# Kernel optimization log

Measured on AMD Instinct MI355X. Metric: run time of the kernel, lower is better.

Reference implementation:

```python
import jax, jax.numpy as jnp
import numpy as np

T_STEPS = 4000          # T_ms / dt = 1000 / 0.25
N_IN, N_OUT = 64, 10
HID = [1024, 1024]
DT, TAU = 0.25, 10.0
BETA = float(np.exp(-DT / TAU))   # beta_snn
THR = 1.0                          # thr_snn
SLOPE = 1.0                        # spike_snn uses slope=1.0
W_STD = 32.0                       # W_STD_CUBA

@jax.custom_vjp
def spike(u):
    # SurrogateSpike.forward: heaviside on (mem - thr)
    return (u >= 0).astype(u.dtype)

def _spike_fwd(u):
    return spike(u), u

def _spike_bwd(u, g):
    # fast-sigmoid surrogate: slope / (1 + slope*|u|)^2
    grad = SLOPE / (1.0 + SLOPE * jnp.abs(u)) ** 2
    return (g * grad,)

spike.defvjp(_spike_fwd, _spike_bwd)

def setup_inputs() -> dict:
    key = jax.random.key(0)
    ks = jax.random.split(key, 8)
    B = 16
    # Bernoulli(0.05) input spike train, time-major [T, B, N_IN]
    input_spikes = (jax.random.uniform(ks[0], (T_STEPS, B, N_IN)) < 0.05).astype(jnp.float32)
    sizes = [N_IN] + HID + [N_OUT]
    inp = {"input_spikes": input_spikes}
    for i, (n_pre, n_post) in enumerate(zip(sizes[:-1], sizes[1:])):
        # init_weight 'normal': clamp(N(0, W_STD), min=0) / n_pre
        w = jnp.maximum(jax.random.normal(ks[i + 1], (n_pre, n_post)) * W_STD, 0.0) / n_pre
        inp[f"W{i}"] = w.astype(jnp.float32)
        inp[f"b{i}"] = jnp.zeros((n_post,), jnp.float32)
    return inp

def reference(input_spikes, W0, b0, W1, b1, W2, b2):
    # Dale's law: feedforward weights clamped >= 0 in forward
    Ws = [jnp.maximum(W, 0.0) for W in (W0, W1, W2)]
    bs = [b0, b1, b2]
    B = input_spikes.shape[1]
    sizes = HID + [N_OUT]
    mems0 = tuple(jnp.zeros((B, n), input_spikes.dtype) for n in sizes)

    def step(mems, s_in):
        s = s_in
        new_mems = []
        for l in range(len(Ws)):
            I = s @ Ws[l] + bs[l]                 # [B, n_post]
            m = BETA * mems[l] + I                # LIF decay + drive
            sp = spike(m - THR)                   # surrogate-grad spike
            m = jnp.where(sp > 0, 0.0, m)         # hard reset to zero
            new_mems.append(m)
            s = sp
        return tuple(new_mems), s                 # emit output-layer spikes

    _, out_spikes = jax.lax.scan(step, mems0, input_spikes)
    return out_spikes  # [T, B, N_OUT]
```

## Files before the change

### kernel.cpp

```cpp
#include <hip/hip_runtime.h>
#include <hip/hip_bf16.h>
#include <math.h>


#define T_STEPS 4000
#define NB 16
#define N_IN 64
#define NH 1024
#define N_OUT 10
#define SEGO 40
#define SEGH 40

typedef __attribute__((ext_vector_type(8))) short bf16x8;
typedef __attribute__((ext_vector_type(4))) float f32x4;
typedef __hip_bfloat16 bf16;
typedef unsigned long long u64;

#define ASG(p) (const __attribute__((address_space(1))) void*)(p)
#define ASL(p) (__attribute__((address_space(3))) void*)(p)


__global__ __launch_bounds__(256) void k_prep(
    const float* __restrict__ in_sp, u64* __restrict__ mask,
    const float* __restrict__ W1, bf16* __restrict__ BT1,
    const float* __restrict__ W2, bf16* __restrict__ BT2,
    float* __restrict__ mst, int nM, int ZB, int MB) {
    __shared__ float Wlds[64][65];
    int b = blockIdx.x;
    const int tid = threadIdx.x;
    if (b < ZB) {
        int i = b * 256 + tid;
        if (i < nM) mst[i] = 0.f;
        return;
    }
    b -= ZB;
    if (b < MB) {
        int w = b * 4 + (tid >> 6);
        int lane = tid & 63;
        float v = in_sp[(size_t)w * 64 + lane];
        u64 bal = __ballot(v > 0.5f);
        if (lane == 0) mask[w] = bal;
        return;
    }
    b -= MB;
    if (b < 256) {
        const int lane = tid & 63;
        const int wr   = tid >> 6;
        const int k0 = (b & 15) * 64;
        const int n0 = (b >> 4) * 64;
#pragma unroll
        for (int rr = 0; rr < 16; ++rr) {
            int kl = wr * 16 + rr;
            Wlds[kl][lane] = W1[(size_t)(k0 + kl) * 1024 + n0 + lane];
        }
        __syncthreads();
#pragma unroll
        for (int rr = 0; rr < 16; ++rr) {
            int nl = wr * 16 + rr;
            float w = fmaxf(Wlds[lane][nl], 0.f);
            bf16 h = __float2bfloat16(w);
            float hf = __bfloat162float(h);
            bf16 l = __float2bfloat16(w - hf);
            size_t base = (size_t)(n0 + nl) * 2048 + k0 + lane;
            BT1[base] = h;
            BT1[base + 1024] = l;
        }
        return;
    }
    b -= 256;
    {
        int idx = b * 256 + tid;
        int total = 128 * 2 * NH;
        if (idx >= total) return;
        int n  = idx / (2 * NH);
        int k2 = idx - n * (2 * NH);
        int lo = (k2 >= NH);
        int k = lo ? (k2 - NH) : k2;
        float v = 0.f;
        if (n < N_OUT) {
            float w = fmaxf(W2[(size_t)k * N_OUT + n], 0.f);
            float hi = __bfloat162float(__float2bfloat16(w));
            v = lo ? (w - hi) : w;
        }
        BT2[idx] = __float2bfloat16(v);
    }
}

__global__ void k_unpack(const u64* __restrict__ BITS, float* __restrict__ out,
                         int total) {
    int idx = blockIdx.x * 256 + threadIdx.x;
    if (idx >= total) return;
    int t   = idx / (NB * N_OUT);
    int rem = idx - t * (NB * N_OUT);
    int b = rem / N_OUT;
    int k = rem - b * N_OUT;
    u64 w = BITS[(size_t)(t / SEGO) * 256 + b * 16 + k];
    out[idx] = ((w >> (t % SEGO)) & 1ULL) ? 1.f : 0.f;
}


__device__ __forceinline__ void scan_out_body(
    const float* __restrict__ I2, const float* __restrict__ bias,
    float* __restrict__ mstate, u64* __restrict__ BITS,
    int Tc, float* seg, int tid) {
    float* segA = seg;
    float* segB = seg + SEGO * 256;
    const bool act = tid < 256;
    const int lane = tid & 63;
    const int wave = tid >> 6;
    const int k = tid & 15;
    float m = 0.f, bj = 0.f;
    if (act) {
        m = mstate[tid];
        bj = (k < N_OUT) ? bias[k] : 0.f;
    }
    const int nseg = Tc / SEGO;

#define O_PREFETCH(SEGBUF, SIDX)                                            \
    if (act) {                                                              \
        const float* src = I2 + (size_t)(SIDX) * SEGO * 256                 \
                              + (size_t)wave * 256 + lane * 4;              \
        _Pragma("unroll")                                                   \
        for (int g = 0; g < SEGO / 4; ++g)                                  \
            __builtin_amdgcn_global_load_lds(                               \
                ASG(src + (size_t)(g * 4) * 256),                           \
                ASL(&SEGBUF[(g * 4 + wave) * 256]), 16, 0, 0);              \
    }

#define O_PROC(SEGBUF, SIDX)                                                \
    if (act) {                                                              \
        u64 obits = 0;                                                      \
        _Pragma("unroll")                                                   \
        for (int sb = 0; sb < SEGO / 8; ++sb) {                             \
            float v[8];                                                     \
            _Pragma("unroll")                                               \
            for (int u = 0; u < 8; ++u)                                     \
                v[u] = SEGBUF[(sb * 8 + u) * 256 + tid];                    \
            _Pragma("unroll")                                               \
            for (int u = 0; u < 8; ++u) {                                   \
                m = fmaf(beta_c, m, v[u] + bj);                             \
                bool sp = (m >= 1.0f);                                      \
                obits |= ((u64)(sp ? 1 : 0)) << (sb * 8 + u);               \
                m = sp ? 0.f : m;                                           \
            }                                                               \
        }                                                                   \
        BITS[(size_t)(SIDX) * 256 + tid] = obits;                           \
    }

    const float beta_c = 0.97530991202833261687f;
    O_PREFETCH(segA, 0);
    O_PREFETCH(segB, 1);
    asm volatile("s_waitcnt vmcnt(10)" ::: "memory");
    __builtin_amdgcn_sched_barrier(0);
    __builtin_amdgcn_s_barrier();
    for (int s = 0; s < nseg; s += 2) {
        O_PROC(segA, s);
        if (s + 2 < nseg) {
            O_PREFETCH(segA, s + 2);
            asm volatile("s_waitcnt vmcnt(11)" ::: "memory");
        } else {
            asm volatile("s_waitcnt vmcnt(1)" ::: "memory");
        }
        __builtin_amdgcn_sched_barrier(0);
        __builtin_amdgcn_s_barrier();
        O_PROC(segB, s + 1);
        if (s + 3 < nseg) {
            O_PREFETCH(segB, s + 3);
            asm volatile("s_waitcnt vmcnt(11)" ::: "memory");
            __builtin_amdgcn_sched_barrier(0);
            __builtin_amdgcn_s_barrier();
        } else if (s + 2 < nseg) {
            asm volatile("s_waitcnt vmcnt(1)" ::: "memory");
            __builtin_amdgcn_sched_barrier(0);
            __builtin_amdgcn_s_barrier();
        }
    }
    if (act) mstate[tid] = m;
#undef O_PREFETCH
#undef O_PROC
}

__global__ __launch_bounds__(256) void k_scan_out(
    const float* __restrict__ I2, const float* __restrict__ bias,
    float* __restrict__ mstate, u64* __restrict__ BITS, int Tc) {
    __shared__ __align__(16) float seg[2 * SEGO * 256];
    scan_out_body(I2, bias, mstate, BITS, Tc, seg, threadIdx.x);
}


__global__ __launch_bounds__(256) void k_gemm_thin(
    const bf16* __restrict__ A, const bf16* __restrict__ BT,
    float* __restrict__ C) {
    const int tid  = threadIdx.x;
    const int lane = tid & 63;
    const int wave = tid >> 6;
    const int r16 = lane & 15;
    const int kg  = lane >> 4;
    const int m0 = blockIdx.x * 64 + wave * 16;
    f32x4 acc = {};
    const bf16* ap = A + (size_t)(m0 + r16) * 1024 + kg * 8;
    const bf16* bh = BT + (size_t)r16 * 2048 + kg * 8;
    const bf16* bl = bh + 1024;
#pragma unroll 8
    for (int kt = 0; kt < 32; ++kt) {
        const int ka = kt * 32;
        bf16x8 af  = *(const bf16x8*)(ap + ka);
        bf16x8 bfh = *(const bf16x8*)(bh + ka);
        bf16x8 bfl = *(const bf16x8*)(bl + ka);
        acc = __builtin_amdgcn_mfma_f32_16x16x32_bf16(af, bfh, acc, 0, 0, 0);
        acc = __builtin_amdgcn_mfma_f32_16x16x32_bf16(af, bfl, acc, 0, 0, 0);
    }
#pragma unroll
    for (int rr = 0; rr < 4; ++rr)
        C[(size_t)(m0 + kg * 4 + rr) * 16 + r16] = acc[rr];
}


__global__ __launch_bounds__(512) void k_gemm8(
    const bf16* __restrict__ A, const bf16* __restrict__ BT,
    float* __restrict__ C, int gx,
    const float* __restrict__ I2t, const float* __restrict__ b2t,
    float* __restrict__ m2t, u64* __restrict__ BITSt, int tcT, int doTail) {
    __shared__ __align__(16) char LDS[131072];
    const int tid  = threadIdx.x;

    if (doTail && (int)blockIdx.x == (int)gridDim.x - 1) {
        scan_out_body(I2t, b2t, m2t, BITSt, tcT, (float*)LDS, tid);
        return;
    }

    const int KA = 1024, K2 = 2048;
    const int kmask = KA - 1;
    const int nwg = gridDim.x - doTail;
    const int wg  = blockIdx.x;
    const int q = nwg >> 3, r = nwg & 7;
    const int xcd = wg & 7, idx0 = wg >> 3;
    const int swz = (xcd < r ? xcd * (q + 1) : r * (q + 1) + (xcd - r) * q) + idx0;
    const int gy = nwg / gx;
    const int n0 = (swz % gy) * 256;
    const int m0 = (swz / gy) * 256;

    const int lane = tid & 63;
    const int wave = tid >> 6;
    const int wm = (wave >> 2) * 128;
    const int wn = (wave & 3) * 64;
    const int r16l = lane & 15;
    const int kg   = lane >> 4;
    const int hA   = wave >> 2;
    const int hB   = (wave & 3) >> 1;
    const int wn64 = wave & 1;

    const int po = (r16l * 64 + kg * 16) ^ (((r16l >> 3) & 1) << 5);
    const char* bA[2] = { LDS + hA * 16384 + po,
                          LDS + 65536 + hA * 16384 + po };
    const char* bB[2] = { LDS + 32768 + hB * 16384 + po,
                          LDS + 98304 + hB * 16384 + po };
    const int bOff = wn64 * 8192;

    int s_row[2], s_col[2];
#pragma unroll
    for (int rr = 0; rr < 2; ++rr) {
        int d = (rr * 512 + tid) * 16;
        int l = d ^ (((d >> 9) & 1) << 5);
        int sub = l >> 10;
        int w = l & 1023;
        s_row[rr] = (sub >> 1) * 16 + (w >> 6);
        s_col[rr] = ((sub & 1) * 64 + (w & 63)) >> 1;
    }

#define HBASE(BUF, OP, HALF) ((((BUF) * 2 + (OP)) * 2 + (HALF)) * 16384)
#define STAGE_A(BUF, HALF, K0)                                              \
    {                                                                       \
        _Pragma("unroll")                                                   \
        for (int rr = 0; rr < 2; ++rr)                                      \
            __builtin_amdgcn_global_load_lds(                               \
                ASG(A + (size_t)(m0 + (HALF) * 128 + s_row[rr]) * KA        \
                    + (((K0) + s_col[rr]) & kmask)),                        \
                ASL(LDS + HBASE(BUF, 0, HALF) + (rr * 512 + wave * 64) * 16), \
                16, 0, 0);                                                  \
    }
#define STAGE_B(BUF, HALF, K0)                                              \
    {                                                                       \
        _Pragma("unroll")                                                   \
        for (int rr = 0; rr < 2; ++rr)                                      \
            __builtin_amdgcn_global_load_lds(                               \
                ASG(BT + (size_t)(n0 + (HALF) * 128 + s_row[rr]) * K2       \
                    + (K0) + s_col[rr]),                                    \
                ASL(LDS + HBASE(BUF, 1, HALF) + (rr * 512 + wave * 64) * 16), \
                16, 0, 0);                                                  \
    }

    f32x4 acc[8][4] = {};
    bf16x8 a[4][2], b[4][2];

#define MM(MIB, NIB)                                                        \
    {                                                                       \
        _Pragma("unroll")                                                   \
        for (int i = 0; i < 4; ++i)                                         \
            _Pragma("unroll")                                               \
            for (int j = 0; j < 2; ++j) {                                   \
                acc[(MIB) + i][(NIB) + j] =                                 \
                    __builtin_amdgcn_mfma_f32_16x16x32_bf16(                \
                        a[i][0], b[(NIB) + j][0], acc[(MIB) + i][(NIB) + j], 0, 0, 0); \
                acc[(MIB) + i][(NIB) + j] =                                 \
                    __builtin_amdgcn_mfma_f32_16x16x32_bf16(                \
                        a[i][1], b[(NIB) + j][1], acc[(MIB) + i][(NIB) + j], 0, 0, 0); \
            }                                                               \
    }

#define PH_SYNC()                                                           \
    __builtin_amdgcn_s_barrier();                                           \
    asm volatile("s_waitcnt lgkmcnt(0)" ::: "memory");                      \
    __builtin_amdgcn_sched_barrier(0);

#define KTILE(BUF, SK)                                                      \
    {                                                                       \
        _Pragma("unroll")                                                   \
        for (int i = 0; i < 4; ++i) {                                       \
            a[i][0] = *(const bf16x8*)(bA[BUF] + i * 2048);                 \
            a[i][1] = *(const bf16x8*)(bA[BUF] + i * 2048 + 1024);          \
        }                                                                   \
        _Pragma("unroll")                                                   \
        for (int j = 0; j < 2; ++j) {                                       \
            b[j][0] = *(const bf16x8*)(bB[BUF] + bOff + j * 2048);          \
            b[j][1] = *(const bf16x8*)(bB[BUF] + bOff + j * 2048 + 1024);   \
        }                                                                   \
        PH_SYNC();                                                          \
        __builtin_amdgcn_s_setprio(1);                                      \
        MM(0, 0);                                                           \
        __builtin_amdgcn_s_setprio(0);                                      \
        __builtin_amdgcn_s_barrier();                                       \
        _Pragma("unroll")                                                   \
        for (int j = 0; j < 2; ++j) {                                       \
            b[2 + j][0] = *(const bf16x8*)(bB[BUF] + bOff + (2 + j) * 2048); \
            b[2 + j][1] = *(const bf16x8*)(bB[BUF] + bOff + (2 + j) * 2048 + 1024); \
        }                                                                   \
        PH_SYNC();                                                          \
        __builtin_amdgcn_s_setprio(1);                                      \
        MM(0, 2);                                                           \
        __builtin_amdgcn_s_setprio(0);                                      \
        __builtin_amdgcn_s_barrier();                                       \
        _Pragma("unroll")                                                   \
        for (int i = 0; i < 4; ++i) {                                       \
            a[i][0] = *(const bf16x8*)(bA[BUF] + (4 + i) * 2048);           \
            a[i][1] = *(const bf16x8*)(bA[BUF] + (4 + i) * 2048 + 1024);    \
        }                                                                   \
        STAGE_B(BUF, 0, SK);                                                \
        STAGE_B(BUF, 1, SK);                                                \
        PH_SYNC();                                                          \
        __builtin_amdgcn_s_setprio(1);                                      \
        MM(4, 0);                                                           \
        __builtin_amdgcn_s_setprio(0);                                      \
        __builtin_amdgcn_s_barrier();                                       \
        STAGE_A(BUF, 0, SK);                                                \
        STAGE_A(BUF, 1, SK);                                                \
        PH_SYNC();                                                          \
        __builtin_amdgcn_s_setprio(1);                                      \
        MM(4, 2);                                                           \
        __builtin_amdgcn_s_setprio(0);                                      \
        asm volatile("s_waitcnt vmcnt(8)" ::: "memory");                    \
        __builtin_amdgcn_sched_barrier(0);                                  \
        __builtin_amdgcn_s_barrier();                                       \
    }

    STAGE_A(0, 0, 0);  STAGE_A(0, 1, 0);  STAGE_B(0, 0, 0);  STAGE_B(0, 1, 0);
    STAGE_A(1, 0, 64); STAGE_A(1, 1, 64); STAGE_B(1, 0, 64); STAGE_B(1, 1, 64);
    asm volatile("s_waitcnt vmcnt(8)" ::: "memory");
    __builtin_amdgcn_sched_barrier(0);
    __builtin_amdgcn_s_barrier();

    for (int it = 0; it < 16; ++it) {
        const int k0  = it * 128;
        const int ksA = (k0 + 128) & (K2 - 1);
        const int ksB = (k0 + 192) & (K2 - 1);
        KTILE(0, ksA);
        KTILE(1, ksB);
    }
    asm volatile("s_waitcnt vmcnt(0)" ::: "memory");
    __builtin_amdgcn_sched_barrier(0);

#pragma unroll
    for (int mi = 0; mi < 8; ++mi)
#pragma unroll
        for (int ni = 0; ni < 4; ++ni)
#pragma unroll
            for (int rr = 0; rr < 4; ++rr) {
                int row = m0 + wm + mi * 16 + kg * 4 + rr;
                int col = n0 + wn + ni * 16 + r16l;
                C[(size_t)row * 1024 + col] = acc[mi][ni][rr];
            }
#undef KTILE
#undef PH_SYNC
#undef MM
#undef STAGE_A
#undef STAGE_B
#undef HBASE
}


__global__ __launch_bounds__(64) void k_scan_l0(
    const u64* __restrict__ mask,
    const float* __restrict__ W0,
    const float* __restrict__ bias,
    float* __restrict__ mstate, bf16* __restrict__ S, int Tc, float beta) {
    __shared__ float Ilds[2][16][68];
    const int lane = threadIdx.x;
    const int gid  = blockIdx.x * 64 + lane;
    const int b  = blockIdx.x >> 4;
    const int q  = blockIdx.x & 15;
    const int j0 = q * 64;
    const int r16 = lane & 15;
    const int kg  = lane >> 4;
    bf16x8 bh[4][2], bl[4][2];
#pragma unroll
    for (int jt = 0; jt < 4; ++jt)
#pragma unroll
        for (int kk = 0; kk < 2; ++kk)
#pragma unroll
            for (int e = 0; e < 8; ++e) {
                int k = kk * 32 + kg * 8 + e;
                float w = fmaxf(W0[(size_t)k * 1024 + j0 + jt * 16 + r16], 0.f);
                bf16 h = __float2bfloat16(w);
                float hf = __bfloat162float(h);
                bf16 l = __float2bfloat16(w - hf);
                bh[jt][kk][e] = *(short*)&h;
                bl[jt][kk][e] = *(short*)&l;
            }
    float m = mstate[gid];
    const float bj = bias[j0 + lane];
    const size_t stride = (size_t)NB * NH;
    const int ntile = Tc / 16;
    const int tmax = ntile - 1;

#define LOADM(TT) mask[(size_t)(((TT) <= tmax ? (TT) : tmax) * 16 + r16) * NB + b]

#define L0_COMPUTE(MSK, P)                                                  \
    {                                                                       \
        f32x4 acc[4] = {};                                                  \
        _Pragma("unroll")                                                   \
        for (int kk = 0; kk < 2; ++kk) {                                    \
            unsigned byte8 = (unsigned)(((MSK) >> (kk * 32 + kg * 8)) & 0xFF); \
            bf16x8 af;                                                      \
            _Pragma("unroll")                                               \
            for (int e = 0; e < 8; ++e)                                     \
                af[e] = ((byte8 >> e) & 1) ? (short)0x3F80 : (short)0;      \
            _Pragma("unroll")                                               \
            for (int jt = 0; jt < 4; ++jt) {                                \
                acc[jt] = __builtin_amdgcn_mfma_f32_16x16x32_bf16(          \
                    af, bh[jt][kk], acc[jt], 0, 0, 0);                      \
                acc[jt] = __builtin_amdgcn_mfma_f32_16x16x32_bf16(          \
                    af, bl[jt][kk], acc[jt], 0, 0, 0);                      \
            }                                                               \
        }                                                                   \
        _Pragma("unroll")                                                   \
        for (int jt = 0; jt < 4; ++jt)                                      \
            _Pragma("unroll")                                               \
            for (int rr = 0; rr < 4; ++rr)                                  \
                Ilds[P][kg * 4 + rr][jt * 16 + r16] = acc[jt][rr];          \
    }

    u64 mc = LOADM(0);
    L0_COMPUTE(mc, 0);
    u64 mn = LOADM(1);
    for (int tt = 0; tt < ntile; ++tt) {
        __builtin_amdgcn_s_barrier();
        float v[16];
#pragma unroll
        for (int u = 0; u < 16; ++u)
            v[u] = Ilds[tt & 1][u][lane];
        u64 m2 = LOADM(tt + 2);
        if (tt + 1 < ntile) L0_COMPUTE(mn, (tt + 1) & 1);
        unsigned short o[16];
#pragma unroll
        for (int u = 0; u < 16; ++u) {
            m = fmaf(beta, m, v[u] + bj);
            bool sp = (m >= 1.0f);
            o[u] = sp ? (unsigned short)0x3F80 : (unsigned short)0;
            m = sp ? 0.f : m;
        }
#pragma unroll
        for (int u = 0; u < 16; ++u)
            ((unsigned short*)S)[(size_t)(tt * 16 + u) * stride + gid] = o[u];
        mn = m2;
    }
    mstate[gid] = m;
#undef L0_COMPUTE
#undef LOADM
}

__global__ __launch_bounds__(64) void k_scan_hidden(
    const float* __restrict__ I, const float* __restrict__ bias,
    float* __restrict__ mstate, bf16* __restrict__ S, int Tc, float beta) {
    __shared__ __align__(16) float segA[SEGH * 64];
    __shared__ __align__(16) float segB[SEGH * 64];
    const int lane = threadIdx.x;
    const int gid  = blockIdx.x * 64 + lane;
    const int j = gid & (NH - 1);
    float m = mstate[gid];
    const float bj = bias[j];
    const size_t stride = (size_t)NB * NH;
    const int nseg = Tc / SEGH;
    const int lrow = lane >> 4;
    const int lcol = (lane & 15) << 2;

#define H_PREFETCH(SEGBUF, SIDX)                                            \
    {                                                                       \
        const float* src = I + (size_t)(SIDX) * SEGH * stride               \
                             + (size_t)lrow * stride + blockIdx.x * 64 + lcol; \
        _Pragma("unroll")                                                   \
        for (int g = 0; g < SEGH / 4; ++g)                                  \
            __builtin_amdgcn_global_load_lds(                               \
                ASG(src + (size_t)(g * 4) * stride),                        \
                ASL(&SEGBUF[g * 256]), 16, 0, 0);                           \
    }

#define H_PROC(SEGBUF, SIDX)                                                \
    {                                                                       \
        const int btt = (SIDX) * SEGH;                                      \
        _Pragma("unroll")                                                   \
        for (int sb = 0; sb < SEGH / 8; ++sb) {                             \
            float v[8];                                                     \
            _Pragma("unroll")                                               \
            for (int u = 0; u < 8; ++u)                                     \
                v[u] = SEGBUF[(sb * 8 + u) * 64 + lane];                    \
            unsigned short o[8];                                            \
            _Pragma("unroll")                                               \
            for (int u = 0; u < 8; ++u) {                                   \
                m = fmaf(beta, m, v[u] + bj);                               \
                bool sp = (m >= 1.0f);                                      \
                o[u] = sp ? (unsigned short)0x3F80 : (unsigned short)0;     \
                m = sp ? 0.f : m;                                           \
            }                                                               \
            _Pragma("unroll")                                               \
            for (int u = 0; u < 8; ++u)                                     \
                ((unsigned short*)S)[(size_t)(btt + sb * 8 + u) * stride + gid] = o[u]; \
        }                                                                   \
    }

    H_PREFETCH(segA, 0);
    H_PREFETCH(segB, 1);
    asm volatile("s_waitcnt vmcnt(10)" ::: "memory");
    __builtin_amdgcn_sched_barrier(0);
    for (int s = 0; s < nseg; s += 2) {
        H_PROC(segA, s);
        if (s + 2 < nseg) {
            H_PREFETCH(segA, s + 2);
            asm volatile("s_waitcnt vmcnt(50)" ::: "memory");
        } else {
            asm volatile("s_waitcnt vmcnt(40)" ::: "memory");
        }
        __builtin_amdgcn_sched_barrier(0);
        H_PROC(segB, s + 1);
        if (s + 3 < nseg) {
            H_PREFETCH(segB, s + 3);
            asm volatile("s_waitcnt vmcnt(50)" ::: "memory");
            __builtin_amdgcn_sched_barrier(0);
        } else if (s + 2 < nseg) {
            asm volatile("s_waitcnt vmcnt(40)" ::: "memory");
            __builtin_amdgcn_sched_barrier(0);
        }
    }
    mstate[gid] = m;
#undef H_PREFETCH
#undef H_PROC
}


extern "C" void kernel_launch(void* const* d_in, const int* in_sizes, int n_in,
                              void* d_out, int out_size, void* d_ws, size_t ws_size,
                              hipStream_t stream) {
    const float* in_sp = (const float*)d_in[0];
    const float* W0 = (const float*)d_in[1];
    const float* b0 = (const float*)d_in[2];
    const float* W1 = (const float*)d_in[3];
    const float* b1 = (const float*)d_in[4];
    const float* W2 = (const float*)d_in[5];
    const float* b2 = (const float*)d_in[6];
    float* out = (float*)d_out;

    char* p = (char*)d_ws;
    auto carve = [&](size_t bytes) -> void* {
        char* r = p; p += (bytes + 255) & ~(size_t)255; return (void*)r;
    };
    u64*  MASK  = (u64*)carve((size_t)T_STEPS * NB * 8);
    bf16* BT1   = (bf16*)carve((size_t)NH * 2 * NH * 2);
    bf16* BT2   = (bf16*)carve((size_t)128 * 2 * NH * 2);
    float* m0s  = (float*)carve((size_t)NB * NH * 4);
    float* m1s  = (float*)carve((size_t)NB * NH * 4);
    float* m2s  = (float*)carve((size_t)NB * 16 * 4);
    float* I2BUF = (float*)carve((size_t)T_STEPS * NB * 16 * 4);
    u64*  BITS  = (u64*)carve((size_t)(T_STEPS / SEGO) * 256 * 8);
    size_t fixed = (size_t)(p - (char*)d_ws);

    const int tc_opts[3] = {2000, 800, 400};
    int Tc = 400;
    for (int i = 0; i < 3; ++i) {
        size_t Mc_ = (size_t)tc_opts[i] * NB;
        size_t need = fixed
            + ((Mc_ * NH * 4 + 255) & ~(size_t)255)
            + ((Mc_ * NH * 2 + 255) & ~(size_t)255);
        if (need <= ws_size) { Tc = tc_opts[i]; break; }
    }
    size_t Mc = (size_t)Tc * NB;
    float* IBUF = (float*)carve(Mc * NH * 4);
    bf16*  S    = (bf16*)carve(Mc * NH * 2);

    const float beta = (float)exp(-0.25 / 10.0);

    int nM = NB * NH * 2 + NB * 16;
    const int ZB = (nM + 255) / 256;
    const int MB = (T_STEPS * NB) / 4;
    const int L2B = (128 * 2 * NH + 255) / 256;
    k_prep<<<ZB + MB + 256 + L2B, 256, 0, stream>>>(
        in_sp, MASK, W1, BT1, W2, BT2, m0s, nM, ZB, MB);

    const int C = T_STEPS / Tc;
    const int gx8 = (int)(Mc / 256);
    const int gthin = (int)(Mc / 64);
    for (int c = 0; c < C; ++c) {
        int t0 = c * Tc;
        k_scan_l0<<<256, 64, 0, stream>>>(MASK + (size_t)t0 * NB, W0, b0,
                                          m0s, S, Tc, beta);
        if (c == 0) {
            k_gemm8<<<gx8 * 4, 512, 0, stream>>>(S, BT1, IBUF, gx8,
                                                 nullptr, nullptr, nullptr,
                                                 nullptr, 0, 0);
        } else {
            int tp = (c - 1) * Tc;
            k_gemm8<<<gx8 * 4 + 1, 512, 0, stream>>>(
                S, BT1, IBUF, gx8,
                I2BUF + (size_t)tp * NB * 16, b2, m2s,
                BITS + (size_t)(tp / SEGO) * 256, Tc, 1);
        }
        k_scan_hidden<<<(NB * NH) / 64, 64, 0, stream>>>(IBUF, b1, m1s, S, Tc, beta);
        k_gemm_thin<<<gthin, 256, 0, stream>>>(S, BT2,
                                               I2BUF + (size_t)t0 * NB * 16);
    }
    int tl = (C - 1) * Tc;
    k_scan_out<<<1, 256, 0, stream>>>(I2BUF + (size_t)tl * NB * 16, b2, m2s,
                                      BITS + (size_t)(tl / SEGO) * 256, Tc);
    int nOut = T_STEPS * NB * N_OUT;
    k_unpack<<<(nOut + 255) / 256, 256, 0, stream>>>(BITS, out, nOut);
}
```

Measured before the change: 672.1 us.

## Interleave hi/lo weight K-blocks so each A tile is reused across both halves

The split-bf16 weight matrix is reordered so the hi and lo halves of each 64-wide K block sit next to each other. The GEMM main loop then loads each A tile once into LDS and reuses it for two consecutive B tiles (hi, then lo), instead of reloading A for the second half of K. This roughly halves A-side global-to-LDS traffic. In exchange the LDS buffering scheme and wait counts become more intricate, with separate even and odd k-tile macros.

```diff
diff --git a/kernel.cpp b/kernel.cpp
--- a/kernel.cpp
+++ b/kernel.cpp
@@ -61,9 +61,9 @@
             bf16 h = __float2bfloat16(w);
             float hf = __bfloat162float(h);
             bf16 l = __float2bfloat16(w - hf);
-            size_t base = (size_t)(n0 + nl) * 2048 + k0 + lane;
+            size_t base = (size_t)(n0 + nl) * 2048 + 2 * k0 + lane;
             BT1[base] = h;
-            BT1[base + 1024] = l;
+            BT1[base + 64] = l;
         }
         return;
     }
@@ -229,8 +229,7 @@
         return;
     }
 
-    const int KA = 1024, K2 = 2048;
-    const int kmask = KA - 1;
+    const int KA = 1024;
     const int nwg = gridDim.x - doTail;
     const int wg  = blockIdx.x;
     const int q = nwg >> 3, r = nwg & 7;
@@ -252,8 +251,8 @@
 
     const int po = (r16l * 64 + kg * 16) ^ (((r16l >> 3) & 1) << 5);
     const char* bA[2] = { LDS + hA * 16384 + po,
-                          LDS + 65536 + hA * 16384 + po };
-    const char* bB[2] = { LDS + 32768 + hB * 16384 + po,
+                          LDS + 32768 + hA * 16384 + po };
+    const char* bB[2] = { LDS + 65536 + hB * 16384 + po,
                           LDS + 98304 + hB * 16384 + po };
     const int bOff = wn64 * 8192;
 
@@ -268,15 +267,15 @@
         s_col[rr] = ((sub & 1) * 64 + (w & 63)) >> 1;
     }
 
-#define HBASE(BUF, OP, HALF) ((((BUF) * 2 + (OP)) * 2 + (HALF)) * 16384)
-#define STAGE_A(BUF, HALF, K0)                                              \
+#define STAGE_A(ADST, HALF, K0)                                             \
     {                                                                       \
         _Pragma("unroll")                                                   \
         for (int rr = 0; rr < 2; ++rr)                                      \
             __builtin_amdgcn_global_load_lds(                               \
                 ASG(A + (size_t)(m0 + (HALF) * 128 + s_row[rr]) * KA        \
-                    + (((K0) + s_col[rr]) & kmask)),                        \
-                ASL(LDS + HBASE(BUF, 0, HALF) + (rr * 512 + wave * 64) * 16), \
+                    + (K0) + s_col[rr]),                                    \
+                ASL(LDS + (ADST) * 32768 + (HALF) * 16384                   \
+                    + (rr * 512 + wave * 64) * 16),                         \
                 16, 0, 0);                                                  \
     }
 #define STAGE_B(BUF, HALF, K0)                                              \
@@ -284,9 +283,10 @@
         _Pragma("unroll")                                                   \
         for (int rr = 0; rr < 2; ++rr)                                      \
             __builtin_amdgcn_global_load_lds(                               \
-                ASG(BT + (size_t)(n0 + (HALF) * 128 + s_row[rr]) * K2       \
+                ASG(BT + (size_t)(n0 + (HALF) * 128 + s_row[rr]) * 2048     \
                     + (K0) + s_col[rr]),                                    \
-                ASL(LDS + HBASE(BUF, 1, HALF) + (rr * 512 + wave * 64) * 16), \
+                ASL(LDS + 65536 + (BUF) * 32768 + (HALF) * 16384            \
+                    + (rr * 512 + wave * 64) * 16),                         \
                 16, 0, 0);                                                  \
     }
 
@@ -313,17 +313,17 @@
     asm volatile("s_waitcnt lgkmcnt(0)" ::: "memory");                      \
     __builtin_amdgcn_sched_barrier(0);
 
-#define KTILE(BUF, SK)                                                      \
+#define KT_EVEN(ABUF, BKN, AKN)                                             \
     {                                                                       \
         _Pragma("unroll")                                                   \
         for (int i = 0; i < 4; ++i) {                                       \
-            a[i][0] = *(const bf16x8*)(bA[BUF] + i * 2048);                 \
-            a[i][1] = *(const bf16x8*)(bA[BUF] + i * 2048 + 1024);          \
+            a[i][0] = *(const bf16x8*)(bA[ABUF] + i * 2048);                \
+            a[i][1] = *(const bf16x8*)(bA[ABUF] + i * 2048 + 1024);         \
         }                                                                   \
         _Pragma("unroll")                                                   \
         for (int j = 0; j < 2; ++j) {                                       \
-            b[j][0] = *(const bf16x8*)(bB[BUF] + bOff + j * 2048);          \
-            b[j][1] = *(const bf16x8*)(bB[BUF] + bOff + j * 2048 + 1024);   \
+            b[j][0] = *(const bf16x8*)(bB[0] + bOff + j * 2048);            \
+            b[j][1] = *(const bf16x8*)(bB[0] + bOff + j * 2048 + 1024);     \
         }                                                                   \
         PH_SYNC();                                                          \
         __builtin_amdgcn_s_setprio(1);                                      \
@@ -332,8 +332,8 @@
         __builtin_amdgcn_s_barrier();                                       \
         _Pragma("unroll")                                                   \
         for (int j = 0; j < 2; ++j) {                                       \
-            b[2 + j][0] = *(const bf16x8*)(bB[BUF] + bOff + (2 + j) * 2048); \
-            b[2 + j][1] = *(const bf16x8*)(bB[BUF] + bOff + (2 + j) * 2048 + 1024); \
+            b[2 + j][0] = *(const bf16x8*)(bB[0] + bOff + (2 + j) * 2048);  \
+            b[2 + j][1] = *(const bf16x8*)(bB[0] + bOff + (2 + j) * 2048 + 1024); \
         }                                                                   \
         PH_SYNC();                                                          \
         __builtin_amdgcn_s_setprio(1);                                      \
@@ -342,18 +342,18 @@
         __builtin_amdgcn_s_barrier();                                       \
         _Pragma("unroll")                                                   \
         for (int i = 0; i < 4; ++i) {                                       \
-            a[i][0] = *(const bf16x8*)(bA[BUF] + (4 + i) * 2048);           \
-            a[i][1] = *(const bf16x8*)(bA[BUF] + (4 + i) * 2048 + 1024);    \
-        }                                                                   \
-        STAGE_B(BUF, 0, SK);                                                \
-        STAGE_B(BUF, 1, SK);                                                \
+            a[i][0] = *(const bf16x8*)(bA[ABUF] + (4 + i) * 2048);          \
+            a[i][1] = *(const bf16x8*)(bA[ABUF] + (4 + i) * 2048 + 1024);   \
+        }                                                                   \
+        STAGE_B(0, 0, BKN);                                                 \
+        STAGE_B(0, 1, BKN);                                                 \
         PH_SYNC();                                                          \
         __builtin_amdgcn_s_setprio(1);                                      \
         MM(4, 0);                                                           \
         __builtin_amdgcn_s_setprio(0);                                      \
         __builtin_amdgcn_s_barrier();                                       \
-        STAGE_A(BUF, 0, SK);                                                \
-        STAGE_A(BUF, 1, SK);                                                \
+        STAGE_A((ABUF) ^ 1, 0, AKN);                                        \
+        STAGE_A((ABUF) ^ 1, 1, AKN);                                        \
         PH_SYNC();                                                          \
         __builtin_amdgcn_s_setprio(1);                                      \
         MM(4, 2);                                                           \
@@ -363,18 +363,70 @@
         __builtin_amdgcn_s_barrier();                                       \
     }
 
-    STAGE_A(0, 0, 0);  STAGE_A(0, 1, 0);  STAGE_B(0, 0, 0);  STAGE_B(0, 1, 0);
-    STAGE_A(1, 0, 64); STAGE_A(1, 1, 64); STAGE_B(1, 0, 64); STAGE_B(1, 1, 64);
-    asm volatile("s_waitcnt vmcnt(8)" ::: "memory");
+#define KT_ODD(ABUF, BKN)                                                   \
+    {                                                                       \
+        _Pragma("unroll")                                                   \
+        for (int i = 0; i < 4; ++i) {                                       \
+            a[i][0] = *(const bf16x8*)(bA[ABUF] + i * 2048);                \
+            a[i][1] = *(const bf16x8*)(bA[ABUF] + i * 2048 + 1024);         \
+        }                                                                   \
+        _Pragma("unroll")                                                   \
+        for (int j = 0; j < 2; ++j) {                                       \
+            b[j][0] = *(const bf16x8*)(bB[1] + bOff + j * 2048);            \
+            b[j][1] = *(const bf16x8*)(bB[1] + bOff + j * 2048 + 1024);     \
+        }                                                                   \
+        PH_SYNC();                                                          \
+        __builtin_amdgcn_s_setprio(1);                                      \
+        MM(0, 0);                                                           \
+        __builtin_amdgcn_s_setprio(0);                                      \
+        __builtin_amdgcn_s_barrier();                                       \
+        _Pragma("unroll")                                                   \
+        for (int j = 0; j < 2; ++j) {                                       \
+            b[2 + j][0] = *(const bf16x8*)(bB[1] + bOff + (2 + j) * 2048);  \
+            b[2 + j][1] = *(const bf16x8*)(bB[1] + bOff + (2 + j) * 2048 + 1024); \
+        }                                                                   \
+        PH_SYNC();                                                          \
+        __builtin_amdgcn_s_setprio(1);                                      \
+        MM(0, 2);                                                           \
+        __builtin_amdgcn_s_setprio(0);                                      \
+        __builtin_amdgcn_s_barrier();                                       \
+        _Pragma("unroll")                                                   \
+        for (int i = 0; i < 4; ++i) {                                       \
+            a[i][0] = *(const bf16x8*)(bA[ABUF] + (4 + i) * 2048);          \
+            a[i][1] = *(const bf16x8*)(bA[ABUF] + (4 + i) * 2048 + 1024);   \
+        }                                                                   \
+        STAGE_B(1, 0, BKN);                                                 \
+        STAGE_B(1, 1, BKN);                                                 \
+        PH_SYNC();                                                          \
+        __builtin_amdgcn_s_setprio(1);                                      \
+        MM(4, 0);                                                           \
+        __builtin_amdgcn_s_setprio(0);                                      \
+        __builtin_amdgcn_s_barrier();                                       \
+        PH_SYNC();                                                          \
+        __builtin_amdgcn_s_setprio(1);                                      \
+        MM(4, 2);                                                           \
+        __builtin_amdgcn_s_setprio(0);                                      \
+        asm volatile("s_waitcnt vmcnt(4)" ::: "memory");                    \
+        __builtin_amdgcn_sched_barrier(0);                                  \
+        __builtin_amdgcn_s_barrier();                                       \
+    }
+
+    STAGE_B(0, 0, 0);  STAGE_B(0, 1, 0);
+    STAGE_A(0, 0, 0);  STAGE_A(0, 1, 0);
+    STAGE_B(1, 0, 64); STAGE_B(1, 1, 64);
+    asm volatile("s_waitcnt vmcnt(4)" ::: "memory");
     __builtin_amdgcn_sched_barrier(0);
     __builtin_amdgcn_s_barrier();
 
-    for (int it = 0; it < 16; ++it) {
-        const int k0  = it * 128;
-        const int ksA = (k0 + 128) & (K2 - 1);
-        const int ksB = (k0 + 192) & (K2 - 1);
-        KTILE(0, ksA);
-        KTILE(1, ksB);
+    for (int it2 = 0; it2 < 16; it2 += 2) {
+        const int ak1 = (64 * (it2 + 1)) & 1023;
+        const int be1 = (128 * (it2 + 1)) & 2047;
+        KT_EVEN(0, be1, ak1);
+        KT_ODD(0, be1 + 64);
+        const int ak2 = (64 * (it2 + 2)) & 1023;
+        const int be2 = (128 * (it2 + 2)) & 2047;
+        KT_EVEN(1, be2, ak2);
+        KT_ODD(1, be2 + 64);
     }
     asm volatile("s_waitcnt vmcnt(0)" ::: "memory");
     __builtin_amdgcn_sched_barrier(0);
@@ -389,12 +441,12 @@
                 int col = n0 + wn + ni * 16 + r16l;
                 C[(size_t)row * 1024 + col] = acc[mi][ni][rr];
             }
-#undef KTILE
+#undef KT_ODD
+#undef KT_EVEN
 #undef PH_SYNC
 #undef MM
 #undef STAGE_A
 #undef STAGE_B
-#undef HBASE
 }
 
 
```

After: 658.5 us. 2.0% less time.
